# Kernel optimization log

Measured on AMD Instinct MI355X. Metric: run time of the kernel, lower is better.

Reference implementation:

```python
import jax, jax.numpy as jnp
import numpy as np

B, T, D, H = 4, 4096, 1024, 4
DK = D // H
DV = D // H
CH = 64           # chunk_size
C = T // CH


def setup_inputs() -> dict:
    key = jax.random.key(0)
    ks = jax.random.split(key, 10)
    def w(k, shape, fan_in):
        return jax.random.normal(k, shape, jnp.float32) * (fan_in ** -0.5)
    return {
        "x": jax.random.normal(ks[0], (B, T, D), jnp.float32),
        "Wq": w(ks[1], (D, D), D),
        "Wk": w(ks[2], (D, D), D),
        "Wv": w(ks[3], (D, D), D),
        "Wb": w(ks[4], (D, H), D),      # beta projection
        "Wa": w(ks[5], (D, H), D),      # decay-gate projection
        "A_log": jnp.log(jax.random.uniform(ks[6], (H,), jnp.float32, 1.0, 16.0)),
        "dt_bias": jnp.zeros((H,), jnp.float32),
        "Wg": w(ks[7], (D, D), D),      # output-gate projection
        "norm_w": jnp.ones((DV,), jnp.float32),
        "Wo": w(ks[8], (D, D), D),
    }


def _l2norm(x, eps=1e-6):
    return x * jax.lax.rsqrt(jnp.sum(x * x, axis=-1, keepdims=True) + eps)


def _gdn_forward(x, Wq, Wk, Wv, Wb, Wa, A_log, dt_bias, Wg, norm_w, Wo):
    # projections; q/k L2-normalized per head, q scaled by 1/sqrt(dk)
    q = _l2norm((x @ Wq).reshape(B, T, H, DK)) * (DK ** -0.5)
    k = _l2norm((x @ Wk).reshape(B, T, H, DK))
    v = (x @ Wv).reshape(B, T, H, DV)
    beta = jax.nn.sigmoid(x @ Wb)                                        # [B,T,H]
    dec = jnp.exp(-jnp.exp(A_log) * jax.nn.softplus(x @ Wa + dt_bias))   # [B,T,H] in (0,1)

    # gated delta rule recurrence: S_t = dec_t*S_{t-1} + beta_t * k_t (v_t - k_t^T S_{t-1})
    def step(S, t):
        qt, kt, vt, bt, dt = t                    # [B,H,DK],[B,H,DK],[B,H,DV],[B,H],[B,H]
        S = S * dt[..., None, None]               # gated decay of state [B,H,DK,DV]
        pred = jnp.einsum('bhk,bhkv->bhv', kt, S)
        S = S + kt[..., :, None] * (bt[..., None] * (vt - pred))[..., None, :]
        ot = jnp.einsum('bhk,bhkv->bhv', qt, S)
        return S, ot

    def chunk_fn(S, chunk):
        return jax.lax.scan(step, S, chunk)
    chunk_fn = jax.checkpoint(chunk_fn)           # store only chunk-boundary states

    def to_chunks(a):                              # [B,T,...] -> [C,CH,B,H,...]
        a = jnp.moveaxis(a, 1, 0)
        return a.reshape((C, CH) + a.shape[1:])

    xs = tuple(to_chunks(a) for a in (q, k, v, beta, dec))
    S0 = jnp.zeros((B, H, DK, DV), jnp.float32)
    _, o = jax.lax.scan(chunk_fn, S0, xs)         # o: [C,CH,B,H,DV]
    o = jnp.moveaxis(o.reshape(T, B, H, DV), 0, 1)  # [B,T,H,DV]

    # gated RMSNorm + output projection
    gate = (x @ Wg).reshape(B, T, H, DV)
    o = o * jax.lax.rsqrt(jnp.mean(o * o, axis=-1, keepdims=True) + 1e-5) * norm_w
    o = o * jax.nn.silu(gate)
    return o.reshape(B, T, D) @ Wo


def reference(x, Wq, Wk, Wv, Wb, Wa, A_log, dt_bias, Wg, norm_w, Wo):
    return _gdn_forward(x, Wq, Wk, Wv, Wb, Wa, A_log, dt_bias, Wg, norm_w, Wo)
```

## Files before the change

kernel.cpp:

```cpp
#include <hip/hip_runtime.h>

typedef unsigned short u16;
typedef __bf16 bf16x8 __attribute__((ext_vector_type(8)));
typedef u16 u16x8 __attribute__((ext_vector_type(8)));
typedef u16 u16x4 __attribute__((ext_vector_type(4)));
typedef float f32x4 __attribute__((ext_vector_type(4)));

__device__ __forceinline__ float bf2f(u16 v) {
    union { unsigned u; float f; } c; c.u = ((unsigned)v) << 16; return c.f;
}
__device__ __forceinline__ u16 f2bf_h(float f) {
    __bf16 h = (__bf16)f;
    union { __bf16 h; u16 u; } c; c.h = h; return c.u;
}

__device__ __forceinline__ bf16x8 ldfrag(const u16* base, int stride, int row0, int k0, int lane) {
    return *(const bf16x8*)(base + (size_t)(row0 + (lane & 15)) * stride + k0 + (lane >> 4) * 8);
}

__device__ __forceinline__ void block_barrier() {
    __builtin_amdgcn_sched_barrier(0);
    asm volatile("s_waitcnt lgkmcnt(0)");
    __builtin_amdgcn_s_barrier();
    __builtin_amdgcn_sched_barrier(0);
}

__device__ __forceinline__ void gl2lds16(const void* g, void* l) {
    __builtin_amdgcn_global_load_lds(
        (const __attribute__((address_space(1))) unsigned int*)g,
        (__attribute__((address_space(3))) unsigned int*)l, 16, 0, 0);
}

__global__ __launch_bounds__(256) void cvt_kernel(const float* __restrict__ src,
                                                  u16* __restrict__ dst) {
    const long i = ((long)blockIdx.x * 256 + threadIdx.x) * 4;
    f32x4 v = *(const f32x4*)(src + i);
    u16x4 o;
#pragma unroll
    for (int r = 0; r < 4; r++) o[r] = f2bf_h(v[r]);
    *(u16x4*)(dst + i) = o;
}

__global__ __launch_bounds__(256) void transpose_kernel(const float* __restrict__ src,
                                                        u16* __restrict__ dst) {
    __shared__ float tile[32][33];
    const int n0 = blockIdx.x * 32, k0 = blockIdx.y * 32;
    const int tx = threadIdx.x, ty = threadIdx.y;
#pragma unroll
    for (int i = 0; i < 32; i += 8)
        tile[ty + i][tx] = src[(long)(k0 + ty + i) * 1024 + n0 + tx];
    __syncthreads();
#pragma unroll
    for (int i = 0; i < 32; i += 8)
        dst[(long)(n0 + ty + i) * 1024 + k0 + tx] = f2bf_h(tile[tx][ty + i]);
}

template <int F32OUT>
__global__ __launch_bounds__(256) void gemm_kernel(const u16* __restrict__ A,
                                                   const u16* __restrict__ BT,
                                                   void* __restrict__ Cv,
                                                   int M, int N, int K, int ldc) {
    __shared__ __attribute__((aligned(16))) u16 As[128][32];
    __shared__ __attribute__((aligned(16))) u16 Bs[128][32];
    const int tid  = threadIdx.x;
    const int lane = tid & 63;
    const int wave = tid >> 6;
    const int wm   = (wave >> 1) * 64;
    const int wn   = (wave & 1) * 64;
    const long m0  = (long)blockIdx.y * 128;
    const long n0  = (long)blockIdx.x * 128;

    const f32x4 zero = {0.f, 0.f, 0.f, 0.f};
    f32x4 acc[4][4];
#pragma unroll
    for (int i = 0; i < 4; i++)
#pragma unroll
        for (int j = 0; j < 4; j++) acc[i][j] = zero;

    const int r0 = tid >> 2;
    const int c0 = (tid & 3) * 8;
    const u16* Ag = A + (m0 + r0) * K + c0;
    const u16* Bg = BT + (n0 + r0) * K + c0;
    u16* AsW  = &As[wave * 16][0];
    u16* AsW2 = &As[wave * 16 + 64][0];
    u16* BsW  = &Bs[wave * 16][0];
    u16* BsW2 = &Bs[wave * 16 + 64][0];

    for (int k0 = 0; k0 < K; k0 += 32) {
        gl2lds16(Ag + k0, AsW);
        gl2lds16(Ag + (long)64 * K + k0, AsW2);
        gl2lds16(Bg + k0, BsW);
        gl2lds16(Bg + (long)64 * K + k0, BsW2);
        __syncthreads();
        const int qk = (lane >> 4) * 8;
        const int mr = lane & 15;
        bf16x8 af[4], bfr[4];
#pragma unroll
        for (int i = 0; i < 4; i++) af[i]  = *(const bf16x8*)(&As[wm + i * 16 + mr][qk]);
#pragma unroll
        for (int j = 0; j < 4; j++) bfr[j] = *(const bf16x8*)(&Bs[wn + j * 16 + mr][qk]);
#pragma unroll
        for (int i = 0; i < 4; i++)
#pragma unroll
            for (int j = 0; j < 4; j++)
                acc[i][j] = __builtin_amdgcn_mfma_f32_16x16x32_bf16(af[i], bfr[j], acc[i][j], 0, 0, 0);
        __syncthreads();
    }

    const int cr = (lane >> 4) * 4;
    const int cc = lane & 15;
#pragma unroll
    for (int i = 0; i < 4; i++) {
#pragma unroll
        for (int j = 0; j < 4; j++) {
            const long m = m0 + wm + i * 16 + cr;
            const long n = n0 + wn + j * 16 + cc;
            if (F32OUT) {
                float* C = (float*)Cv;
#pragma unroll
                for (int r = 0; r < 4; r++) C[(m + r) * ldc + n] = acc[i][j][r];
            } else {
                u16* C = (u16*)Cv;
#pragma unroll
                for (int r = 0; r < 4; r++) C[(m + r) * ldc + n] = f2bf_h(acc[i][j][r]);
            }
        }
    }
}

#define LDA 40

__global__ __launch_bounds__(256) void gemm_a32_kernel(const float* __restrict__ A,
                                                       const u16* __restrict__ BT,
                                                       u16* __restrict__ C,
                                                       int M, int N, int K, int ldc) {
    __shared__ __attribute__((aligned(16))) u16 As[128][LDA];
    __shared__ __attribute__((aligned(16))) u16 Bs[128][32];
    const int tid  = threadIdx.x;
    const int lane = tid & 63;
    const int wave = tid >> 6;
    const int wm   = (wave >> 1) * 64;
    const int wn   = (wave & 1) * 64;
    const long m0  = (long)blockIdx.y * 128;
    const long n0  = (long)blockIdx.x * 128;

    const f32x4 zero = {0.f, 0.f, 0.f, 0.f};
    f32x4 acc[4][4];
#pragma unroll
    for (int i = 0; i < 4; i++)
#pragma unroll
        for (int j = 0; j < 4; j++) acc[i][j] = zero;

    const int r0 = tid >> 2;
    const int c0 = (tid & 3) * 8;
    const float* Ag = A + (m0 + r0) * K + c0;
    const u16* Bg = BT + (n0 + r0) * K + c0;
    u16* BsW  = &Bs[wave * 16][0];
    u16* BsW2 = &Bs[wave * 16 + 64][0];

    for (int k0 = 0; k0 < K; k0 += 32) {
        gl2lds16(Bg + k0, BsW);
        gl2lds16(Bg + (long)64 * K + k0, BsW2);
        f32x4 af0 = *(const f32x4*)(Ag + k0);
        f32x4 af1 = *(const f32x4*)(Ag + k0 + 4);
        f32x4 ag0 = *(const f32x4*)(Ag + (long)64 * K + k0);
        f32x4 ag1 = *(const f32x4*)(Ag + (long)64 * K + k0 + 4);
        u16x8 a0, a1;
#pragma unroll
        for (int r = 0; r < 4; r++) {
            a0[r] = f2bf_h(af0[r]); a0[r + 4] = f2bf_h(af1[r]);
            a1[r] = f2bf_h(ag0[r]); a1[r + 4] = f2bf_h(ag1[r]);
        }
        *(u16x8*)(&As[r0][c0])      = a0;
        *(u16x8*)(&As[r0 + 64][c0]) = a1;
        __syncthreads();
        const int qk = (lane >> 4) * 8;
        const int mr = lane & 15;
        bf16x8 af[4], bfr[4];
#pragma unroll
        for (int i = 0; i < 4; i++) af[i]  = *(const bf16x8*)(&As[wm + i * 16 + mr][qk]);
#pragma unroll
        for (int j = 0; j < 4; j++) bfr[j] = *(const bf16x8*)(&Bs[wn + j * 16 + mr][qk]);
#pragma unroll
        for (int i = 0; i < 4; i++)
#pragma unroll
            for (int j = 0; j < 4; j++)
                acc[i][j] = __builtin_amdgcn_mfma_f32_16x16x32_bf16(af[i], bfr[j], acc[i][j], 0, 0, 0);
        __syncthreads();
    }

    const int cr = (lane >> 4) * 4;
    const int cc = lane & 15;
#pragma unroll
    for (int i = 0; i < 4; i++) {
#pragma unroll
        for (int j = 0; j < 4; j++) {
            const long m = m0 + wm + i * 16 + cr;
            const long n = n0 + wn + j * 16 + cc;
#pragma unroll
            for (int r = 0; r < 4; r++) C[(m + r) * ldc + n] = f2bf_h(acc[i][j][r]);
        }
    }
}

__global__ __launch_bounds__(1024) void norm_beta_kernel(
    const u16* __restrict__ xb, u16* __restrict__ Y,
    const float* __restrict__ Wb, const float* __restrict__ Wa,
    const float* __restrict__ A_log, const float* __restrict__ dt_bias,
    float* __restrict__ beta, float* __restrict__ dec) {
    const long row = blockIdx.x;
    const int c = threadIdx.x;
    const int h = c >> 8;
    float qv = bf2f(Y[row * 3072 + c]);
    float kv = bf2f(Y[row * 3072 + 1024 + c]);
    float xv = bf2f(xb[row * 1024 + c]);
    float vals[10];
    vals[0] = qv * qv;
    vals[1] = kv * kv;
#pragma unroll
    for (int hh = 0; hh < 4; hh++) vals[2 + hh] = xv * Wb[c * 4 + hh];
#pragma unroll
    for (int hh = 0; hh < 4; hh++) vals[6 + hh] = xv * Wa[c * 4 + hh];
#pragma unroll
    for (int i = 0; i < 10; i++)
        for (int off = 32; off; off >>= 1) vals[i] += __shfl_xor(vals[i], off, 64);

    __shared__ float wred[16][10];
    __shared__ float sQ[4], sK[4];
    const int w = c >> 6;
    if ((c & 63) == 0) {
#pragma unroll
        for (int i = 0; i < 10; i++) wred[w][i] = vals[i];
    }
    __syncthreads();
    if (c < 4) {
        float s = wred[c * 4 + 0][0] + wred[c * 4 + 1][0] + wred[c * 4 + 2][0] + wred[c * 4 + 3][0];
        sQ[c] = rsqrtf(s + 1e-6f) * 0.0625f;
    } else if (c < 8) {
        int hh = c - 4;
        float s = wred[hh * 4 + 0][1] + wred[hh * 4 + 1][1] + wred[hh * 4 + 2][1] + wred[hh * 4 + 3][1];
        sK[hh] = rsqrtf(s + 1e-6f);
    } else if (c < 12) {
        int hh = c - 8;
        float s = 0.f;
        for (int ww = 0; ww < 16; ww++) s += wred[ww][2 + hh];
        beta[row * 4 + hh] = 1.f / (1.f + expf(-s));
    } else if (c < 16) {
        int hh = c - 12;
        float s = 0.f;
        for (int ww = 0; ww < 16; ww++) s += wred[ww][6 + hh];
        float z = s + dt_bias[hh];
        float sp = (z > 0.f) ? (z + log1pf(expf(-z))) : log1pf(expf(z));
        dec[row * 4 + hh] = expf(-expf(A_log[hh]) * sp);
    }
    __syncthreads();
    Y[row * 3072 + c]        = f2bf_h(qv * sQ[h]);
    Y[row * 3072 + 1024 + c] = f2bf_h(kv * sK[h]);
}

__global__ __launch_bounds__(256) void prep_kernel(const u16* __restrict__ Y,
                                                   const float* __restrict__ beta,
                                                   const float* __restrict__ dec,
                                                   u16* __restrict__ Tg,
                                                   u16* __restrict__ Mg,
                                                   float* __restrict__ sfg) {
    __shared__ __attribute__((aligned(16))) u16 lds[38400];
    __shared__ float sf[320];
    u16* KS  = lds;
    u16* QS  = lds + 16896;
    u16* AM  = lds + 33792;
    u16* Tm  = lds;
    u16* AMT = lds + 4608;
    u16* MP  = lds + 9216;
    u16* MPT = lds + 13824;

    const int bx = blockIdx.x;
    const int bh = bx >> 6, c = bx & 63;
    const int b = bh >> 2, h = bh & 3;
    const int tid = threadIdx.x, lane = tid & 63, wv = tid >> 6;
    const int quad = lane >> 4, l15 = lane & 15;
    const int tld = tid >> 2, seg = tid & 3;
    const long bt0 = (long)b * 4096 + c * 64;
    u16* Tc = Tg + (size_t)(bh * 64 + c) * 4096;
    u16* Mc = Mg + (size_t)(bh * 64 + c) * 4096;
    const f32x4 z4 = {0.f, 0.f, 0.f, 0.f};

    {
        const long rb = (bt0 + tld) * 3072 + h * 256 + seg * 64;
#pragma unroll
        for (int i = 0; i < 8; i++) {
            *(u16x8*)&KS[tld * 264 + seg * 64 + i * 8] = *(const u16x8*)&Y[rb + 1024 + i * 8];
            *(u16x8*)&QS[tld * 264 + seg * 64 + i * 8] = *(const u16x8*)&Y[rb + i * 8];
        }
    }
    if (wv == 0) {
        float d   = dec [(bt0 + lane) * 4 + h];
        float bt_ = beta[(bt0 + lane) * 4 + h];
        float lg = log2f(fmaxf(d, 1e-30f));
#pragma unroll
        for (int off = 1; off < 64; off <<= 1) {
            float o = __shfl_up(lg, off, 64);
            if (lane >= off) lg += o;
        }
        sf[lane] = lg; sf[192 + lane] = bt_;
        float lgL = __shfl(lg, 63, 64);
        float g = exp2f(lg);
        float* sfc = sfg + (size_t)(bh * 64 + c) * 256;
        sfc[lane]       = g;
        sfc[64 + lane]  = bt_ * g;
        sfc[128 + lane] = bt_;
        sfc[192 + lane] = exp2f(lgL - lg);
    }
    __syncthreads();

    {
        const u16* Ab = (wv < 2) ? KS : QS;
        const int mb = (wv & 1) * 32;
        f32x4 g[2][4];
#pragma unroll
        for (int mi = 0; mi < 2; mi++)
#pragma unroll
            for (int sj = 0; sj < 4; sj++) g[mi][sj] = z4;
#pragma unroll 2
        for (int k0 = 0; k0 < 256; k0 += 32) {
            bf16x8 bfr[4];
#pragma unroll
            for (int sj = 0; sj < 4; sj++) bfr[sj] = ldfrag(KS, 264, sj * 16, k0, lane);
#pragma unroll
            for (int mi = 0; mi < 2; mi++) {
                bf16x8 af = ldfrag(Ab, 264, mb + mi * 16, k0, lane);
#pragma unroll
                for (int sj = 0; sj < 4; sj++)
                    g[mi][sj] = __builtin_amdgcn_mfma_f32_16x16x32_bf16(af, bfr[sj], g[mi][sj], 0, 0, 0);
            }
        }
#pragma unroll
        for (int mi = 0; mi < 2; mi++)
#pragma unroll
            for (int sj = 0; sj < 4; sj++)
#pragma unroll
                for (int r = 0; r < 4; r++) {
                    const int t_ = mb + mi * 16 + quad * 4 + r, s_ = sj * 16 + l15;
                    if (wv < 2)
                        AM[t_ * 72 + s_] = (s_ < t_) ? f2bf_h(sf[192 + t_] * exp2f(sf[t_] - sf[s_]) * g[mi][sj][r]) : (u16)0;
                    else
                        Mc[t_ * 64 + s_] = (s_ <= t_) ? f2bf_h(exp2f(sf[t_] - sf[s_]) * g[mi][sj][r]) : (u16)0;
                }
    }
    __syncthreads();

    {
        const int t_ = tid >> 2;
#pragma unroll
        for (int i = 0; i < 16; i++) {
            const int s_ = (tid & 3) * 16 + i;
            const u16 a = AM[t_ * 72 + s_];
            Tm[t_ * 72 + s_] = (t_ == s_) ? (u16)0x3F80 : (u16)(a ^ 0x8000);
            AMT[s_ * 72 + t_] = a;
        }
    }
    __syncthreads();

    {
        f32x4 sq[4];
#pragma unroll
        for (int sj = 0; sj < 4; sj++) sq[sj] = z4;
#pragma unroll
        for (int k0 = 0; k0 < 64; k0 += 32) {
            bf16x8 a = ldfrag(AM, 72, 16 * wv, k0, lane);
#pragma unroll
            for (int sj = 0; sj < 4; sj++) {
                bf16x8 bb = ldfrag(AMT, 72, sj * 16, k0, lane);
                sq[sj] = __builtin_amdgcn_mfma_f32_16x16x32_bf16(a, bb, sq[sj], 0, 0, 0);
            }
        }
#pragma unroll
        for (int sj = 0; sj < 4; sj++)
#pragma unroll
            for (int r = 0; r < 4; r++) {
                const int t_ = 16 * wv + quad * 4 + r, s_ = sj * 16 + l15;
                const u16 vbf = f2bf_h(sq[sj][r]);
                MP[t_ * 72 + s_] = vbf;
                MPT[s_ * 72 + t_] = vbf;
            }
        __syncthreads();
    }

#pragma unroll 1
    for (int jj = 0; jj < 5; jj++) {
        const bool last = (jj == 4);
        f32x4 pp[4], sq[4];
#pragma unroll
        for (int sj = 0; sj < 4; sj++) {
            sq[sj] = z4;
#pragma unroll
            for (int r = 0; r < 4; r++)
                pp[sj][r] = bf2f(Tm[(16 * wv + quad * 4 + r) * 72 + sj * 16 + l15]);
        }
#pragma unroll
        for (int k0 = 0; k0 < 64; k0 += 32) {
            bf16x8 at = ldfrag(Tm, 72, 16 * wv, k0, lane);
            bf16x8 am = ldfrag(MP, 72, 16 * wv, k0, lane);
#pragma unroll
            for (int sj = 0; sj < 4; sj++) {
                bf16x8 bb = ldfrag(MPT, 72, sj * 16, k0, lane);
                pp[sj] = __builtin_amdgcn_mfma_f32_16x16x32_bf16(at, bb, pp[sj], 0, 0, 0);
                if (!last) sq[sj] = __builtin_amdgcn_mfma_f32_16x16x32_bf16(am, bb, sq[sj], 0, 0, 0);
            }
        }
        __syncthreads();
#pragma unroll
        for (int sj = 0; sj < 4; sj++)
#pragma unroll
            for (int r = 0; r < 4; r++) {
                const int t_ = 16 * wv + quad * 4 + r, s_ = sj * 16 + l15;
                Tm[t_ * 72 + s_] = f2bf_h(pp[sj][r]);
                if (!last) {
                    const u16 vbf = f2bf_h(sq[sj][r]);
                    MP[t_ * 72 + s_] = vbf;
                    MPT[s_ * 72 + t_] = vbf;
                }
            }
        __syncthreads();
    }

    {
        const int t_ = tid >> 2;
#pragma unroll
        for (int i = 0; i < 16; i++) {
            const int s_ = (tid & 3) * 16 + i;
            Tc[t_ * 64 + s_] = Tm[t_ * 72 + s_];
        }
    }
}

struct Frag { bf16x8 f[8]; };

__global__ __launch_bounds__(512, 2) void scan_kernel(const u16* __restrict__ Y,
                                                      const float* __restrict__ sfg,
                                                      const u16* __restrict__ Tg,
                                                      const u16* __restrict__ Mg,
                                                      u16* __restrict__ Ob) {
    __shared__ __attribute__((aligned(16))) u16 KT[4 * 4616];
    __shared__ __attribute__((aligned(16))) u16 ST[64 * 264];
    __shared__ __attribute__((aligned(16))) u16 RHST[64 * 72];
    __shared__ __attribute__((aligned(16))) u16 UTp[64 * 72];
    __shared__ __attribute__((aligned(16))) u16 UTk[64 * 72];

    const int px = blockIdx.x;
    const int bh = (px & 7) | ((px >> 5) << 3);
    const int dvs = (px >> 3) & 3;
    const int b = bh >> 2, h = bh & 3;
    const int tid = threadIdx.x, lane = tid & 63, wv = tid >> 6;
    const int wq = wv & 3;
    const int isQ = wv >> 2;
    const int quad = lane >> 4, l15 = lane & 15;
    const int tW = 16 * wq + l15;
    const int tph = 16 * ((wq + quad) & 3) + l15;
    int toff[4];
#pragma unroll
    for (int j = 0; j < 4; j++) toff[j] = ((((j << 1) + (l15 >> 3)) & 3) << 4);
    const f32x4 z4 = {0.f, 0.f, 0.f, 0.f};

    f32x4 Sacc[2][4];
#pragma unroll
    for (int i = 0; i < 2; i++)
#pragma unroll
        for (int j = 0; j < 4; j++) Sacc[i][j] = z4;
    for (int i = tid; i < 64 * 264; i += 512) ST[i] = 0;
    __syncthreads();

    const long roleOff = isQ ? 0 : 1024;
    Frag F0, F1;
    {
        const u16* Pg = Y + ((long)b * 4096) * 3072 + roleOff + h * 256;
#pragma unroll
        for (int i = 0; i < 8; i++) F0.f[i] = ldfrag(Pg, 3072, 16 * wq, i * 32, lane);
    }

    f32x4 oaccP[4];
#pragma unroll
    for (int j = 0; j < 4; j++) oaccP[j] = z4;
    bf16x8 amP0 = {}, amP1 = {};
    long obP = 0;
    int havePrev = 0;

    auto body = [&](Frag& cur, Frag& nxt, int c) {
        const long bt0 = (long)b * 4096 + (long)c * 64;
        const int cn = (c < 63) ? c + 1 : 63;

        {
            const u16* Pg = Y + ((long)b * 4096 + (long)cn * 64) * 3072 + roleOff + h * 256;
#pragma unroll
            for (int i = 0; i < 8; i++) nxt.f[i] = ldfrag(Pg, 3072, 16 * wq, i * 32, lane);
        }

        const u16* Tc = Tg + (size_t)(bh * 64 + c) * 4096;
        bf16x8 at0 = ldfrag(Tc, 64, 16 * wq, 0, lane);
        bf16x8 at1 = ldfrag(Tc, 64, 16 * wq, 32, lane);
        const float* sfc = sfg + (size_t)(bh * 64 + c) * 256;
        const float gam_l = sfc[tW];
        const float bg_l  = sfc[64 + tW];
        const float bet_l = sfc[128 + tW];
        const float ksc_l = sfc[192 + tW];
        const float gL    = sfc[63];

        u16x4 v4[4];
        if (!isQ) {
            const u16* Vr = Y + (bt0 + tW) * 3072 + 2048 + h * 256 + dvs * 64;
#pragma unroll
            for (int j = 0; j < 4; j++) v4[j] = *(const u16x4*)(Vr + j * 16 + quad * 4);
        } else {
            const u16* Mc = Mg + (size_t)(bh * 64 + c) * 4096;
            bf16x8 amN0 = ldfrag(Mc, 64, 16 * wq, 0, lane);
            bf16x8 amN1 = ldfrag(Mc, 64, 16 * wq, 32, lane);
            if (havePrev) {
#pragma unroll
                for (int sj = 0; sj < 4; sj++) {
                    bf16x8 ua0 = ldfrag(UTp, 72, sj * 16, 0, lane);
                    oaccP[sj] = __builtin_amdgcn_mfma_f32_16x16x32_bf16(ua0, amP0, oaccP[sj], 0, 0, 0);
                    bf16x8 ua1 = ldfrag(UTp, 72, sj * 16, 32, lane);
                    oaccP[sj] = __builtin_amdgcn_mfma_f32_16x16x32_bf16(ua1, amP1, oaccP[sj], 0, 0, 0);
                }
#pragma unroll
                for (int sj = 0; sj < 4; sj++) {
                    u16x4 o4;
#pragma unroll
                    for (int r = 0; r < 4; r++) o4[r] = f2bf_h(oaccP[sj][r]);
                    *(u16x4*)(Ob + obP + sj * 16 + quad * 4) = o4;
                }
            }
            amP0 = amN0; amP1 = amN1;
        }

        f32x4 p[4];
#pragma unroll
        for (int j = 0; j < 4; j++) p[j] = z4;
#pragma unroll
        for (int i = 0; i < 8; i++) {
            bf16x8 sfr[4];
#pragma unroll
            for (int j = 0; j < 4; j++) sfr[j] = ldfrag(ST, 264, j * 16, i * 32, lane);
#pragma unroll
            for (int j = 0; j < 4; j++)
                p[j] = __builtin_amdgcn_mfma_f32_16x16x32_bf16(sfr[j], cur.f[i], p[j], 0, 0, 0);
        }

        if (!isQ) {
#pragma unroll
            for (int i = 0; i < 8; i++) {
                const u16* src = (const u16*)&cur.f[i];
                u16* dst = KT + (i >> 1) * 4616 + ((i & 1) * 32 + quad * 8) * 72 + tph;
#pragma unroll
                for (int jj = 0; jj < 8; jj++) dst[jj * 72] = src[jj];
            }
#pragma unroll
            for (int j = 0; j < 4; j++)
#pragma unroll
                for (int r = 0; r < 4; r++) {
                    const int row = j * 16 + quad * 4 + r;
                    RHST[row * 72 + tW] = f2bf_h(bet_l * bf2f(v4[j][r]) - bg_l * p[j][r]);
                }
        } else {
#pragma unroll
            for (int j = 0; j < 4; j++)
#pragma unroll
                for (int r = 0; r < 4; r++) oaccP[j][r] = gam_l * p[j][r];
            obP = (bt0 + tW) * 1024 + h * 256 + (long)dvs * 64;
            havePrev = 1;
        }
        block_barrier();

        {
#pragma unroll
            for (int s2 = 0; s2 < 2; s2++) {
                const int sj = isQ * 2 + s2;
                f32x4 uu = z4;
                bf16x8 ra0 = ldfrag(RHST, 72, sj * 16, 0, lane);
                uu = __builtin_amdgcn_mfma_f32_16x16x32_bf16(ra0, at0, uu, 0, 0, 0);
                bf16x8 ra1 = ldfrag(RHST, 72, sj * 16, 32, lane);
                uu = __builtin_amdgcn_mfma_f32_16x16x32_bf16(ra1, at1, uu, 0, 0, 0);
#pragma unroll
                for (int r = 0; r < 4; r++) {
                    const int row = sj * 16 + quad * 4 + r;
                    UTp[row * 72 + tW] = f2bf_h(uu[r]);
                    UTk[row * 72 + tW] = f2bf_h(ksc_l * uu[r]);
                }
            }
        }
        block_barrier();

        {
#pragma unroll
            for (int i = 0; i < 2; i++)
#pragma unroll
                for (int j = 0; j < 4; j++) Sacc[i][j] *= gL;
            const u16* KTp = KT + wq * 4616;
#pragma unroll
            for (int k0 = 0; k0 < 64; k0 += 32) {
                bf16x8 au[2], bk[4];
#pragma unroll
                for (int i = 0; i < 2; i++) au[i] = ldfrag(UTk, 72, isQ * 32 + i * 16, k0, lane);
#pragma unroll
                for (int j = 0; j < 4; j++)
                    bk[j] = *(const bf16x8*)(KTp + (size_t)(j * 16 + l15) * 72 +
                                             ((k0 + quad * 8 + toff[j]) & 63));
#pragma unroll
                for (int i = 0; i < 2; i++)
#pragma unroll
                    for (int j = 0; j < 4; j++)
                        Sacc[i][j] = __builtin_amdgcn_mfma_f32_16x16x32_bf16(au[i], bk[j], Sacc[i][j], 0, 0, 0);
            }
#pragma unroll
            for (int i = 0; i < 2; i++)
#pragma unroll
                for (int j = 0; j < 4; j++)
#pragma unroll
                    for (int r = 0; r < 4; r++)
                        ST[(isQ * 32 + i * 16 + quad * 4 + r) * 264 + wq * 64 + j * 16 + l15] = f2bf_h(Sacc[i][j][r]);
        }
        block_barrier();
    };

#pragma unroll 1
    for (int c = 0; c < 64; c += 2) {
        body(F0, F1, c);
        body(F1, F0, c + 1);
    }

    if (isQ) {
#pragma unroll
        for (int sj = 0; sj < 4; sj++) {
            bf16x8 ua0 = ldfrag(UTp, 72, sj * 16, 0, lane);
            oaccP[sj] = __builtin_amdgcn_mfma_f32_16x16x32_bf16(ua0, amP0, oaccP[sj], 0, 0, 0);
            bf16x8 ua1 = ldfrag(UTp, 72, sj * 16, 32, lane);
            oaccP[sj] = __builtin_amdgcn_mfma_f32_16x16x32_bf16(ua1, amP1, oaccP[sj], 0, 0, 0);
        }
#pragma unroll
        for (int sj = 0; sj < 4; sj++) {
            u16x4 o4;
#pragma unroll
            for (int r = 0; r < 4; r++) o4[r] = f2bf_h(oaccP[sj][r]);
            *(u16x4*)(Ob + obP + sj * 16 + quad * 4) = o4;
        }
    }
}

__global__ __launch_bounds__(256) void gate_norm_kernel(const u16* __restrict__ O,
                                                        u16* __restrict__ G,
                                                        const float* __restrict__ norm_w) {
    const long row = blockIdx.x >> 2;
    const int h = blockIdx.x & 3;
    const int dv = threadIdx.x;
    const long idx = row * 1024 + h * 256 + dv;
    float o = bf2f(O[idx]);
    float s = o * o;
#pragma unroll
    for (int off = 32; off; off >>= 1) s += __shfl_xor(s, off, 64);
    __shared__ float wsum[4];
    if ((dv & 63) == 0) wsum[dv >> 6] = s;
    __syncthreads();
    const float tot = wsum[0] + wsum[1] + wsum[2] + wsum[3];
    const float r = rsqrtf(tot * (1.f / 256.f) + 1e-5f);
    const float g = bf2f(G[idx]);
    const float val = o * r * norm_w[dv] * (g / (1.f + expf(-g)));
    G[idx] = f2bf_h(val);
}

extern "C" void kernel_launch(void* const* d_in, const int* in_sizes, int n_in,
                              void* d_out, int out_size, void* d_ws, size_t ws_size,
                              hipStream_t stream) {
    const float* x       = (const float*)d_in[0];
    const float* Wq      = (const float*)d_in[1];
    const float* Wk      = (const float*)d_in[2];
    const float* Wv      = (const float*)d_in[3];
    const float* Wb      = (const float*)d_in[4];
    const float* Wa      = (const float*)d_in[5];
    const float* A_log   = (const float*)d_in[6];
    const float* dt_bias = (const float*)d_in[7];
    const float* Wg      = (const float*)d_in[8];
    const float* norm_w  = (const float*)d_in[9];
    const float* Wo      = (const float*)d_in[10];

    char* p = (char*)d_ws;
    u16*   WT   = (u16*)p;   p += (size_t)5120 * 1024 * 2;
    u16*   Y    = (u16*)p;   p += (size_t)16384 * 3072 * 2;
    u16*   G    = (u16*)p;   p += (size_t)16384 * 1024 * 2;
    u16*   XO   = (u16*)p;   p += (size_t)16384 * 1024 * 2;
    float* beta = (float*)p; p += (size_t)16384 * 4 * 4;
    float* dec  = (float*)p; p += (size_t)16384 * 4 * 4;

    u16* Tg = G;
    u16* Mg = G + (size_t)1024 * 4096;
    float* sfg = (float*)WT;

    cvt_kernel<<<16384, 256, 0, stream>>>(x, XO);

    dim3 tb(32, 8), tg(32, 32);
    transpose_kernel<<<tg, tb, 0, stream>>>(Wq, WT + (size_t)0 * 1024 * 1024);
    transpose_kernel<<<tg, tb, 0, stream>>>(Wk, WT + (size_t)1 * 1024 * 1024);
    transpose_kernel<<<tg, tb, 0, stream>>>(Wv, WT + (size_t)2 * 1024 * 1024);
    transpose_kernel<<<tg, tb, 0, stream>>>(Wg, WT + (size_t)3 * 1024 * 1024);
    transpose_kernel<<<tg, tb, 0, stream>>>(Wo, WT + (size_t)4 * 1024 * 1024);

    gemm_kernel<0><<<dim3(3072 / 128, 16384 / 128), 256, 0, stream>>>(
        XO, WT, (void*)Y, 16384, 3072, 1024, 3072);

    norm_beta_kernel<<<16384, 1024, 0, stream>>>(XO, Y, Wb, Wa, A_log, dt_bias, beta, dec);

    prep_kernel<<<1024, 256, 0, stream>>>(Y, beta, dec, Tg, Mg, sfg);

    scan_kernel<<<64, 512, 0, stream>>>(Y, sfg, Tg, Mg, XO);

    gemm_a32_kernel<<<dim3(1024 / 128, 16384 / 128), 256, 0, stream>>>(
        x, WT + (size_t)3072 * 1024, G, 16384, 1024, 1024, 1024);

    gate_norm_kernel<<<16384 * 4, 256, 0, stream>>>(XO, G, norm_w);

    gemm_kernel<1><<<dim3(1024 / 128, 16384 / 128), 256, 0, stream>>>(
        G, WT + (size_t)4096 * 1024, d_out, 16384, 1024, 1024, 1024);
}
```

Measured before the change: 996.5 us.

## Overlap gate projection GEMM with the scan by co-launching in one kernel

The scan launch previously used only 64 blocks, leaving most CUs idle while the x@Wg GEMM ran afterwards as a separate kernel. The gate GEMM now lives in the same launch: blocks 64 and up each compute two 128x128 tiles using two 256-thread halves, sharing one union shared-memory buffer with the scan. The GEMM output goes to a new workspace buffer, because G is aliased with the scan's Tg/Mg inputs. The five weight transposes are also merged into a single launch using blockIdx.z. Costs are extra workspace memory and a dependence on scan blocks being dispatched early so the GEMM fills the idle CUs.

```diff
diff --git a/kernel.cpp b/kernel.cpp
--- a/kernel.cpp
+++ b/kernel.cpp
@@ -41,9 +41,16 @@
     *(u16x4*)(dst + i) = o;
 }
 
-__global__ __launch_bounds__(256) void transpose_kernel(const float* __restrict__ src,
-                                                        u16* __restrict__ dst) {
+__global__ __launch_bounds__(256) void transpose5_kernel(const float* __restrict__ s0,
+                                                         const float* __restrict__ s1,
+                                                         const float* __restrict__ s2,
+                                                         const float* __restrict__ s3,
+                                                         const float* __restrict__ s4,
+                                                         u16* __restrict__ dstBase) {
     __shared__ float tile[32][33];
+    const int z = blockIdx.z;
+    const float* src = (z == 0) ? s0 : (z == 1) ? s1 : (z == 2) ? s2 : (z == 3) ? s3 : s4;
+    u16* dst = dstBase + (size_t)z * 1024 * 1024;
     const int n0 = blockIdx.x * 32, k0 = blockIdx.y * 32;
     const int tx = threadIdx.x, ty = threadIdx.y;
 #pragma unroll
@@ -124,81 +131,6 @@
 #pragma unroll
                 for (int r = 0; r < 4; r++) C[(m + r) * ldc + n] = f2bf_h(acc[i][j][r]);
             }
-        }
-    }
-}
-
-#define LDA 40
-
-__global__ __launch_bounds__(256) void gemm_a32_kernel(const float* __restrict__ A,
-                                                       const u16* __restrict__ BT,
-                                                       u16* __restrict__ C,
-                                                       int M, int N, int K, int ldc) {
-    __shared__ __attribute__((aligned(16))) u16 As[128][LDA];
-    __shared__ __attribute__((aligned(16))) u16 Bs[128][32];
-    const int tid  = threadIdx.x;
-    const int lane = tid & 63;
-    const int wave = tid >> 6;
-    const int wm   = (wave >> 1) * 64;
-    const int wn   = (wave & 1) * 64;
-    const long m0  = (long)blockIdx.y * 128;
-    const long n0  = (long)blockIdx.x * 128;
-
-    const f32x4 zero = {0.f, 0.f, 0.f, 0.f};
-    f32x4 acc[4][4];
-#pragma unroll
-    for (int i = 0; i < 4; i++)
-#pragma unroll
-        for (int j = 0; j < 4; j++) acc[i][j] = zero;
-
-    const int r0 = tid >> 2;
-    const int c0 = (tid & 3) * 8;
-    const float* Ag = A + (m0 + r0) * K + c0;
-    const u16* Bg = BT + (n0 + r0) * K + c0;
-    u16* BsW  = &Bs[wave * 16][0];
-    u16* BsW2 = &Bs[wave * 16 + 64][0];
-
-    for (int k0 = 0; k0 < K; k0 += 32) {
-        gl2lds16(Bg + k0, BsW);
-        gl2lds16(Bg + (long)64 * K + k0, BsW2);
-        f32x4 af0 = *(const f32x4*)(Ag + k0);
-        f32x4 af1 = *(const f32x4*)(Ag + k0 + 4);
-        f32x4 ag0 = *(const f32x4*)(Ag + (long)64 * K + k0);
-        f32x4 ag1 = *(const f32x4*)(Ag + (long)64 * K + k0 + 4);
-        u16x8 a0, a1;
-#pragma unroll
-        for (int r = 0; r < 4; r++) {
-            a0[r] = f2bf_h(af0[r]); a0[r + 4] = f2bf_h(af1[r]);
-            a1[r] = f2bf_h(ag0[r]); a1[r + 4] = f2bf_h(ag1[r]);
-        }
-        *(u16x8*)(&As[r0][c0])      = a0;
-        *(u16x8*)(&As[r0 + 64][c0]) = a1;
-        __syncthreads();
-        const int qk = (lane >> 4) * 8;
-        const int mr = lane & 15;
-        bf16x8 af[4], bfr[4];
-#pragma unroll
-        for (int i = 0; i < 4; i++) af[i]  = *(const bf16x8*)(&As[wm + i * 16 + mr][qk]);
-#pragma unroll
-        for (int j = 0; j < 4; j++) bfr[j] = *(const bf16x8*)(&Bs[wn + j * 16 + mr][qk]);
-#pragma unroll
-        for (int i = 0; i < 4; i++)
-#pragma unroll
-            for (int j = 0; j < 4; j++)
-                acc[i][j] = __builtin_amdgcn_mfma_f32_16x16x32_bf16(af[i], bfr[j], acc[i][j], 0, 0, 0);
-        __syncthreads();
-    }
-
-    const int cr = (lane >> 4) * 4;
-    const int cc = lane & 15;
-#pragma unroll
-    for (int i = 0; i < 4; i++) {
-#pragma unroll
-        for (int j = 0; j < 4; j++) {
-            const long m = m0 + wm + i * 16 + cr;
-            const long n = n0 + wn + j * 16 + cc;
-#pragma unroll
-            for (int r = 0; r < 4; r++) C[(m + r) * ldc + n] = f2bf_h(acc[i][j][r]);
         }
     }
 }
@@ -435,23 +367,102 @@
 }
 
 struct Frag { bf16x8 f[8]; };
-
-__global__ __launch_bounds__(512, 2) void scan_kernel(const u16* __restrict__ Y,
-                                                      const float* __restrict__ sfg,
-                                                      const u16* __restrict__ Tg,
-                                                      const u16* __restrict__ Mg,
-                                                      u16* __restrict__ Ob) {
-    __shared__ __attribute__((aligned(16))) u16 KT[4 * 4616];
-    __shared__ __attribute__((aligned(16))) u16 ST[64 * 264];
-    __shared__ __attribute__((aligned(16))) u16 RHST[64 * 72];
-    __shared__ __attribute__((aligned(16))) u16 UTp[64 * 72];
-    __shared__ __attribute__((aligned(16))) u16 UTk[64 * 72];
+#define LDA 40
+
+__global__ __launch_bounds__(512, 2) void scan_gate_kernel(
+    const u16* __restrict__ Y, const float* __restrict__ sfg,
+    const u16* __restrict__ Tg, const u16* __restrict__ Mg,
+    u16* __restrict__ Ob,
+    const float* __restrict__ x, const u16* __restrict__ WgT,
+    u16* __restrict__ GX) {
+    __shared__ __attribute__((aligned(16))) u16 smem[49184];
+
+    const int tid = threadIdx.x;
+
+    if (blockIdx.x >= 64) {
+        u16* As = smem + (tid >> 8) * 9216;
+        u16* Bs = As + 5120;
+        const int t256 = tid & 255;
+        const int lane = t256 & 63;
+        const int wave = t256 >> 6;
+        const int wm   = (wave >> 1) * 64;
+        const int wn   = (wave & 1) * 64;
+        const int tl   = (blockIdx.x - 64) * 2 + (tid >> 8);
+        const long m0  = (long)(tl >> 3) * 128;
+        const long n0  = (long)(tl & 7) * 128;
+        const int K = 1024, ldc = 1024;
+
+        const f32x4 zero = {0.f, 0.f, 0.f, 0.f};
+        f32x4 acc[4][4];
+#pragma unroll
+        for (int i = 0; i < 4; i++)
+#pragma unroll
+            for (int j = 0; j < 4; j++) acc[i][j] = zero;
+
+        const int r0 = t256 >> 2;
+        const int c0 = (t256 & 3) * 8;
+        const float* Ag = x + (m0 + r0) * K + c0;
+        const u16* Bg = WgT + (n0 + r0) * K + c0;
+        u16* BsW  = Bs + wave * 16 * 32;
+        u16* BsW2 = Bs + (wave * 16 + 64) * 32;
+
+        for (int k0 = 0; k0 < K; k0 += 32) {
+            gl2lds16(Bg + k0, BsW);
+            gl2lds16(Bg + (long)64 * K + k0, BsW2);
+            f32x4 af0 = *(const f32x4*)(Ag + k0);
+            f32x4 af1 = *(const f32x4*)(Ag + k0 + 4);
+            f32x4 ag0 = *(const f32x4*)(Ag + (long)64 * K + k0);
+            f32x4 ag1 = *(const f32x4*)(Ag + (long)64 * K + k0 + 4);
+            u16x8 a0, a1;
+#pragma unroll
+            for (int r = 0; r < 4; r++) {
+                a0[r] = f2bf_h(af0[r]); a0[r + 4] = f2bf_h(af1[r]);
+                a1[r] = f2bf_h(ag0[r]); a1[r + 4] = f2bf_h(ag1[r]);
+            }
+            *(u16x8*)(As + r0 * LDA + c0)        = a0;
+            *(u16x8*)(As + (r0 + 64) * LDA + c0) = a1;
+            __syncthreads();
+            const int qk = (lane >> 4) * 8;
+            const int mr = lane & 15;
+            bf16x8 af[4], bfr[4];
+#pragma unroll
+            for (int i = 0; i < 4; i++) af[i]  = *(const bf16x8*)(As + (wm + i * 16 + mr) * LDA + qk);
+#pragma unroll
+            for (int j = 0; j < 4; j++) bfr[j] = *(const bf16x8*)(Bs + (wn + j * 16 + mr) * 32 + qk);
+#pragma unroll
+            for (int i = 0; i < 4; i++)
+#pragma unroll
+                for (int j = 0; j < 4; j++)
+                    acc[i][j] = __builtin_amdgcn_mfma_f32_16x16x32_bf16(af[i], bfr[j], acc[i][j], 0, 0, 0);
+            __syncthreads();
+        }
+
+        const int cr = (lane >> 4) * 4;
+        const int cc = lane & 15;
+#pragma unroll
+        for (int i = 0; i < 4; i++) {
+#pragma unroll
+            for (int j = 0; j < 4; j++) {
+                const long m = m0 + wm + i * 16 + cr;
+                const long n = n0 + wn + j * 16 + cc;
+#pragma unroll
+                for (int r = 0; r < 4; r++) GX[(m + r) * ldc + n] = f2bf_h(acc[i][j][r]);
+            }
+        }
+        return;
+    }
+
+    u16* KT   = smem;
+    u16* ST   = smem + 18464;
+    u16* RHST = smem + 35360;
+    u16* UTp  = smem + 39968;
+    u16* UTk  = smem + 44576;
 
     const int px = blockIdx.x;
     const int bh = (px & 7) | ((px >> 5) << 3);
     const int dvs = (px >> 3) & 3;
     const int b = bh >> 2, h = bh & 3;
-    const int tid = threadIdx.x, lane = tid & 63, wv = tid >> 6;
+    const int lane = tid & 63, wv = tid >> 6;
     const int wq = wv & 3;
     const int isQ = wv >> 2;
     const int quad = lane >> 4, l15 = lane & 15;
@@ -689,6 +700,7 @@
     u16*   XO   = (u16*)p;   p += (size_t)16384 * 1024 * 2;
     float* beta = (float*)p; p += (size_t)16384 * 4 * 4;
     float* dec  = (float*)p; p += (size_t)16384 * 4 * 4;
+    u16*   GX   = (u16*)p;   p += (size_t)16384 * 1024 * 2;
 
     u16* Tg = G;
     u16* Mg = G + (size_t)1024 * 4096;
@@ -696,12 +708,8 @@
 
     cvt_kernel<<<16384, 256, 0, stream>>>(x, XO);
 
-    dim3 tb(32, 8), tg(32, 32);
-    transpose_kernel<<<tg, tb, 0, stream>>>(Wq, WT + (size_t)0 * 1024 * 1024);
-    transpose_kernel<<<tg, tb, 0, stream>>>(Wk, WT + (size_t)1 * 1024 * 1024);
-    transpose_kernel<<<tg, tb, 0, stream>>>(Wv, WT + (size_t)2 * 1024 * 1024);
-    transpose_kernel<<<tg, tb, 0, stream>>>(Wg, WT + (size_t)3 * 1024 * 1024);
-    transpose_kernel<<<tg, tb, 0, stream>>>(Wo, WT + (size_t)4 * 1024 * 1024);
+    transpose5_kernel<<<dim3(32, 32, 5), dim3(32, 8), 0, stream>>>(
+        Wq, Wk, Wv, Wg, Wo, WT);
 
     gemm_kernel<0><<<dim3(3072 / 128, 16384 / 128), 256, 0, stream>>>(
         XO, WT, (void*)Y, 16384, 3072, 1024, 3072);
@@ -710,13 +718,11 @@
 
     prep_kernel<<<1024, 256, 0, stream>>>(Y, beta, dec, Tg, Mg, sfg);
 
-    scan_kernel<<<64, 512, 0, stream>>>(Y, sfg, Tg, Mg, XO);
-
-    gemm_a32_kernel<<<dim3(1024 / 128, 16384 / 128), 256, 0, stream>>>(
-        x, WT + (size_t)3072 * 1024, G, 16384, 1024, 1024, 1024);
-
-    gate_norm_kernel<<<16384 * 4, 256, 0, stream>>>(XO, G, norm_w);
+    scan_gate_kernel<<<576, 512, 0, stream>>>(
+        Y, sfg, Tg, Mg, XO, x, WT + (size_t)3072 * 1024, GX);
+
+    gate_norm_kernel<<<16384 * 4, 256, 0, stream>>>(XO, GX, norm_w);
 
     gemm_kernel<1><<<dim3(1024 / 128, 16384 / 128), 256, 0, stream>>>(
-        G, WT + (size_t)4096 * 1024, d_out, 16384, 1024, 1024, 1024);
-}
+        GX, WT + (size_t)4096 * 1024, d_out, 16384, 1024, 1024, 1024);
+}
```

Measured after the change: 898.8 us. 1.11x faster.
